# Kernel optimization log

Hardware: AMD Instinct MI355X
Metric: run time of the kernel (lower is better)

The kernel has to match this reference:

```python
import jax, jax.numpy as jnp
import numpy as np

N = 4096      # num_nodes
E = 16384     # edges per layer view
PHI = 64      # phi_dim
BETA = 0.5
EPS = 1e-8
LM = 1.0      # len(policy) per layer


def _mlp(x, w1, b1, w2, b2):
    # x: [E,1]; Linear(1,PHI) -> ReLU -> Linear(PHI,1)
    h = jax.nn.relu(x * w1[None, :] + b1[None, :])   # [E,PHI]
    return h @ w2[:, None] + b2                      # [E,1]


def setup_inputs() -> dict:
    key = jax.random.key(0)
    ks = jax.random.split(key, 16)
    inp = {
        "A": jax.random.uniform(ks[0], (N, N), dtype=jnp.float32),
        "src0": jax.random.randint(ks[1], (E,), 0, N),
        "dst0": jax.random.randint(ks[2], (E,), 0, N),
        "src1": jax.random.randint(ks[3], (E,), 0, N),
        "dst1": jax.random.randint(ks[4], (E,), 0, N),
        "f0": jax.random.normal(ks[5], (N, 1), dtype=jnp.float32),
        "f1": jax.random.normal(ks[6], (N, 1), dtype=jnp.float32),
        "phi1_w1": jax.random.normal(ks[7], (2, PHI), dtype=jnp.float32) * 0.5,
        "phi1_b1": jax.random.normal(ks[8], (2, PHI), dtype=jnp.float32) * 0.1,
        "phi1_w2": jax.random.normal(ks[9], (2, PHI), dtype=jnp.float32) * 0.5,
        "phi1_b2": jax.random.normal(ks[10], (2,), dtype=jnp.float32) * 0.1,
        "phi2_w1": jax.random.normal(ks[11], (2, PHI), dtype=jnp.float32) * 0.5,
        "phi2_b1": jax.random.normal(ks[12], (2, PHI), dtype=jnp.float32) * 0.1,
        "phi2_w2": jax.random.normal(ks[13], (2, PHI), dtype=jnp.float32) * 0.5,
        "phi2_b2": jax.random.normal(ks[14], (2,), dtype=jnp.float32) * 0.1,
    }
    return inp


def reference(A, src0, dst0, src1, dst1, f0, f1,
              phi1_w1, phi1_b1, phi1_w2, phi1_b2,
              phi2_w1, phi2_b1, phi2_w2, phi2_b2):
    # mean node struct feature across the two merged layer views: [N]
    f_mean = (0.5 * (f0 + f1))[:, 0]
    outs = []
    for lid, (src, dst) in enumerate([(src0, dst0), (src1, dst1)]):
        # gathered, feature-weighted adjacency rows: [E, N]
        mat_src = A[src] * f_mean[None, :]
        mat_dst = A[dst] * f_mean[None, :]
        # diag(mat_src @ mat_dst.T) == per-edge dot product: [E]
        out_struct = jnp.sum(mat_src * mat_dst, axis=-1)
        # random_fill with f_dropout=0 -> deterministic +eps, then row norms
        d_src = jnp.linalg.norm(mat_src + EPS, axis=-1)
        d_dst = jnp.linalg.norm(mat_dst + EPS, axis=-1)
        out_n = (out_struct / (d_src * d_dst))[:, None]      # [E,1]
        y1 = _mlp(out_n, phi1_w1[lid], phi1_b1[lid], phi1_w2[lid], phi1_b2[lid])
        sl1 = BETA * (y1 / LM)
        outs.append(_mlp(sl1, phi2_w1[lid], phi2_b1[lid], phi2_w2[lid], phi2_b2[lid]))
    return tuple(outs)
```

## Files before the change

kernel.cpp:

```cpp
#include <hip/hip_runtime.h>

#define N_NODES 4096
#define EDGES   16384
#define PHI     64
#define EPS_F   1e-8f
#define BETA_F  0.5f
#define NCHUNK  8
#define WCHUNK  512

__device__ __forceinline__ float wave_sum(float v) {
#pragma unroll
    for (int off = 32; off > 0; off >>= 1) v += __shfl_xor(v, off, 64);
    return v;
}

__device__ __forceinline__ unsigned int pack_bf16(float f) {
    unsigned int u = __float_as_uint(f);
    u += 0x7fffu + ((u >> 16) & 1u);
    return u >> 16;
}

__global__ void k_prep(const float* __restrict__ f0, const float* __restrict__ f1,
                       float* __restrict__ fm, float* __restrict__ wsq) {
    int i = blockIdx.x * blockDim.x + threadIdx.x;
    if (i < N_NODES) {
        float m = 0.5f * (f0[i] + f1[i]);
        fm[i]  = m;
        wsq[i] = m * m;
    }
}

__global__ void __launch_bounds__(256) k_rows_fast(const float* __restrict__ A,
                                                   const float* __restrict__ fm,
                                                   unsigned short* __restrict__ B,
                                                   float* __restrict__ dnorm) {
    int row = blockIdx.x;
    const float4* a4  = (const float4*)(A + (size_t)row * N_NODES);
    const float4* fm4 = (const float4*)fm;
    uint2* b2 = (uint2*)(B + (size_t)row * N_NODES);
    int t = threadIdx.x;
    float acc = 0.f;
#pragma unroll
    for (int i = 0; i < 4; ++i) {
        int idx = i * 256 + t;
        float4 a = a4[idx];
        float4 f = fm4[idx];
        float b0 = a.x * f.x, b1 = a.y * f.y, b2v = a.z * f.z, b3 = a.w * f.w;
        float e0 = b0 + EPS_F, e1 = b1 + EPS_F, e2 = b2v + EPS_F, e3 = b3 + EPS_F;
        acc += e0 * e0 + e1 * e1 + e2 * e2 + e3 * e3;
        uint2 p;
        p.x = (pack_bf16(b1) << 16) | pack_bf16(b0);
        p.y = (pack_bf16(b3) << 16) | pack_bf16(b2v);
        b2[idx] = p;
    }
    acc = wave_sum(acc);
    __shared__ float red[4];
    if ((t & 63) == 0) red[t >> 6] = acc;
    __syncthreads();
    if (t == 0) dnorm[row] = sqrtf(red[0] + red[1] + red[2] + red[3]);
}

__global__ void __launch_bounds__(256) k_rows_slow(const float* __restrict__ A,
                                                   const float* __restrict__ fm,
                                                   float* __restrict__ dnorm) {
    int row = blockIdx.x;
    const float4* a4  = (const float4*)(A + (size_t)row * N_NODES);
    const float4* fm4 = (const float4*)fm;
    int t = threadIdx.x;
    float acc = 0.f;
#pragma unroll
    for (int i = 0; i < 4; ++i) {
        int idx = i * 256 + t;
        float4 a = a4[idx];
        float4 f = fm4[idx];
        float e0 = a.x * f.x + EPS_F, e1 = a.y * f.y + EPS_F;
        float e2 = a.z * f.z + EPS_F, e3 = a.w * f.w + EPS_F;
        acc += e0 * e0 + e1 * e1 + e2 * e2 + e3 * e3;
    }
    acc = wave_sum(acc);
    __shared__ float red[4];
    if ((t & 63) == 0) red[t >> 6] = acc;
    __syncthreads();
    if (t == 0) dnorm[row] = sqrtf(red[0] + red[1] + red[2] + red[3]);
}

__device__ __forceinline__ void mlp_epilogue(float x, int lid, int e, int lane,
                                             const float* __restrict__ p1w1, const float* __restrict__ p1b1,
                                             const float* __restrict__ p1w2, const float* __restrict__ p1b2,
                                             const float* __restrict__ p2w1, const float* __restrict__ p2b1,
                                             const float* __restrict__ p2w2, const float* __restrict__ p2b2,
                                             float* __restrict__ out) {
    int wi = lid * PHI + lane;
    float h1 = fmaxf(fmaf(x, p1w1[wi], p1b1[wi]), 0.f);
    float y1 = wave_sum(h1 * p1w2[wi]) + p1b2[lid];
    float sl1 = BETA_F * y1;
    float h2 = fmaxf(fmaf(sl1, p2w1[wi], p2b1[wi]), 0.f);
    float y2 = wave_sum(h2 * p2w2[wi]) + p2b2[lid];
    if (lane == 0) out[lid * EDGES + e] = y2;
}

__global__ void __launch_bounds__(256) k_edges_chunk(
        const unsigned short* __restrict__ B,
        const int* __restrict__ src0, const int* __restrict__ dst0,
        const int* __restrict__ src1, const int* __restrict__ dst1,
        float* __restrict__ P) {
    int blk   = blockIdx.x;
    int chunk = blk & (NCHUNK - 1);
    int slot  = blk >> 3;
    int wave  = threadIdx.x >> 6;
    int lane  = threadIdx.x & 63;
    int ge0   = slot * 16 + wave * 4;
    const unsigned short* Bc = B + (size_t)chunk * WCHUNK;
#pragma unroll
    for (int k = 0; k < 4; ++k) {
        int ge  = ge0 + k;
        int lid = ge >> 14;
        int e   = ge & (EDGES - 1);
        int s = lid ? src1[e] : src0[e];
        int d = lid ? dst1[e] : dst0[e];
        uint4 us = *((const uint4*)(Bc + (size_t)s * N_NODES) + lane);
        uint4 ud = *((const uint4*)(Bc + (size_t)d * N_NODES) + lane);
        float acc = 0.f;
#define ACC_U(U, V)                                                    \
        {                                                              \
            float sl = __uint_as_float((U) << 16);                     \
            float sh = __uint_as_float((U) & 0xffff0000u);             \
            float dl = __uint_as_float((V) << 16);                     \
            float dh = __uint_as_float((V) & 0xffff0000u);             \
            acc = fmaf(sl, dl, acc);                                   \
            acc = fmaf(sh, dh, acc);                                   \
        }
        ACC_U(us.x, ud.x); ACC_U(us.y, ud.y); ACC_U(us.z, ud.z); ACC_U(us.w, ud.w);
#undef ACC_U
        acc = wave_sum(acc);
        if (lane == 0) P[(size_t)ge * NCHUNK + chunk] = acc;
    }
}

__global__ void __launch_bounds__(256) k_finish(
        const float* __restrict__ P, const float* __restrict__ dnorm,
        const int* __restrict__ src0, const int* __restrict__ dst0,
        const int* __restrict__ src1, const int* __restrict__ dst1,
        const float* __restrict__ p1w1, const float* __restrict__ p1b1,
        const float* __restrict__ p1w2, const float* __restrict__ p1b2,
        const float* __restrict__ p2w1, const float* __restrict__ p2b1,
        const float* __restrict__ p2w2, const float* __restrict__ p2b2,
        float* __restrict__ out) {
    int gw   = (int)((blockIdx.x * blockDim.x + threadIdx.x) >> 6);
    int lane = threadIdx.x & 63;
    int lid  = gw >> 14;
    int e    = gw & (EDGES - 1);
    int s = lid ? src1[e] : src0[e];
    int d = lid ? dst1[e] : dst0[e];
    float acc = 0.f;
#pragma unroll
    for (int c = 0; c < NCHUNK; ++c) acc += P[(size_t)gw * NCHUNK + c];
    float x = acc / (dnorm[s] * dnorm[d]);
    mlp_epilogue(x, lid, e, lane, p1w1, p1b1, p1w2, p1b2, p2w1, p2b1, p2w2, p2b2, out);
}

__global__ void __launch_bounds__(256) k_edges_fast(
        const unsigned short* __restrict__ B, const float* __restrict__ dnorm,
        const int* __restrict__ src0, const int* __restrict__ dst0,
        const int* __restrict__ src1, const int* __restrict__ dst1,
        const float* __restrict__ p1w1, const float* __restrict__ p1b1,
        const float* __restrict__ p1w2, const float* __restrict__ p1b2,
        const float* __restrict__ p2w1, const float* __restrict__ p2b1,
        const float* __restrict__ p2w2, const float* __restrict__ p2b2,
        float* __restrict__ out) {
    int gw   = (int)((blockIdx.x * blockDim.x + threadIdx.x) >> 6);
    int lane = threadIdx.x & 63;
    int lid  = gw >> 14;
    int e    = gw & (EDGES - 1);
    int s = lid ? src1[e] : src0[e];
    int d = lid ? dst1[e] : dst0[e];
    const uint4* rs = (const uint4*)(B + (size_t)s * N_NODES);
    const uint4* rd = (const uint4*)(B + (size_t)d * N_NODES);
    float acc = 0.f;
#pragma unroll
    for (int i = 0; i < 8; ++i) {
        uint4 us = rs[i * 64 + lane];
        uint4 ud = rd[i * 64 + lane];
#define ACC_U(U, V)                                                    \
        {                                                              \
            float sl = __uint_as_float((U) << 16);                     \
            float sh = __uint_as_float((U) & 0xffff0000u);             \
            float dl = __uint_as_float((V) << 16);                     \
            float dh = __uint_as_float((V) & 0xffff0000u);             \
            acc = fmaf(sl, dl, acc);                                   \
            acc = fmaf(sh, dh, acc);                                   \
        }
        ACC_U(us.x, ud.x); ACC_U(us.y, ud.y); ACC_U(us.z, ud.z); ACC_U(us.w, ud.w);
#undef ACC_U
    }
    acc = wave_sum(acc);
    float x = acc / (dnorm[s] * dnorm[d]);
    mlp_epilogue(x, lid, e, lane, p1w1, p1b1, p1w2, p1b2, p2w1, p2b1, p2w2, p2b2, out);
}

__global__ void __launch_bounds__(256) k_edges_slow(
        const float* __restrict__ A, const float* __restrict__ wsq,
        const float* __restrict__ dnorm,
        const int* __restrict__ src0, const int* __restrict__ dst0,
        const int* __restrict__ src1, const int* __restrict__ dst1,
        const float* __restrict__ p1w1, const float* __restrict__ p1b1,
        const float* __restrict__ p1w2, const float* __restrict__ p1b2,
        const float* __restrict__ p2w1, const float* __restrict__ p2b1,
        const float* __restrict__ p2w2, const float* __restrict__ p2b2,
        float* __restrict__ out) {
    __shared__ float wl[N_NODES];
    int t = threadIdx.x;
    const float4* w4 = (const float4*)wsq;
    float4* wl4 = (float4*)wl;
    for (int i = t; i < N_NODES / 4; i += 256) wl4[i] = w4[i];
    __syncthreads();

    int gw   = (int)((blockIdx.x * blockDim.x + t) >> 6);
    int lane = t & 63;
    int lid  = gw >> 14;
    int e    = gw & (EDGES - 1);
    int s = lid ? src1[e] : src0[e];
    int d = lid ? dst1[e] : dst0[e];
    const float4* rs = (const float4*)(A + (size_t)s * N_NODES);
    const float4* rd = (const float4*)(A + (size_t)d * N_NODES);
    float acc = 0.f;
#pragma unroll
    for (int i = 0; i < 16; ++i) {
        int idx = i * 64 + lane;
        float4 a = rs[idx];
        float4 b = rd[idx];
        float4 w = wl4[idx];
        acc = fmaf(a.x * b.x, w.x, acc);
        acc = fmaf(a.y * b.y, w.y, acc);
        acc = fmaf(a.z * b.z, w.z, acc);
        acc = fmaf(a.w * b.w, w.w, acc);
    }
    acc = wave_sum(acc);
    float x = acc / (dnorm[s] * dnorm[d]);
    mlp_epilogue(x, lid, e, lane, p1w1, p1b1, p1w2, p1b2, p2w1, p2b1, p2w2, p2b2, out);
}

extern "C" void kernel_launch(void* const* d_in, const int* in_sizes, int n_in,
                              void* d_out, int out_size, void* d_ws, size_t ws_size,
                              hipStream_t stream) {
    const float* A    = (const float*)d_in[0];
    const int*   src0 = (const int*)d_in[1];
    const int*   dst0 = (const int*)d_in[2];
    const int*   src1 = (const int*)d_in[3];
    const int*   dst1 = (const int*)d_in[4];
    const float* f0   = (const float*)d_in[5];
    const float* f1   = (const float*)d_in[6];
    const float* p1w1 = (const float*)d_in[7];
    const float* p1b1 = (const float*)d_in[8];
    const float* p1w2 = (const float*)d_in[9];
    const float* p1b2 = (const float*)d_in[10];
    const float* p2w1 = (const float*)d_in[11];
    const float* p2b1 = (const float*)d_in[12];
    const float* p2w2 = (const float*)d_in[13];
    const float* p2b2 = (const float*)d_in[14];
    float* out = (float*)d_out;

    float* ws  = (float*)d_ws;
    float* fm  = ws;
    float* wsq = ws + N_NODES;
    float* dn  = ws + 2 * N_NODES;
    float* P   = ws + 3 * N_NODES;
    unsigned short* Bnew = (unsigned short*)(P + NCHUNK * 2 * EDGES);
    unsigned short* Bold = (unsigned short*)(ws + 3 * N_NODES);

    size_t need_new = (3ull * N_NODES + (size_t)NCHUNK * 2 * EDGES) * 4
                      + (size_t)N_NODES * N_NODES * 2;
    size_t need_old = 3ull * N_NODES * 4 + (size_t)N_NODES * N_NODES * 2;

    k_prep<<<N_NODES / 256, 256, 0, stream>>>(f0, f1, fm, wsq);
    if (ws_size >= need_new) {
        k_rows_fast<<<N_NODES, 256, 0, stream>>>(A, fm, Bnew, dn);
        k_edges_chunk<<<(2 * EDGES * NCHUNK) / 16, 256, 0, stream>>>(
            Bnew, src0, dst0, src1, dst1, P);
        k_finish<<<(2 * EDGES * 64) / 256, 256, 0, stream>>>(
            P, dn, src0, dst0, src1, dst1,
            p1w1, p1b1, p1w2, p1b2, p2w1, p2b1, p2w2, p2b2, out);
    } else if (ws_size >= need_old) {
        k_rows_fast<<<N_NODES, 256, 0, stream>>>(A, fm, Bold, dn);
        k_edges_fast<<<(2 * EDGES * 64) / 256, 256, 0, stream>>>(
            Bold, dn, src0, dst0, src1, dst1,
            p1w1, p1b1, p1w2, p1b2, p2w1, p2b1, p2w2, p2b2, out);
    } else {
        k_rows_slow<<<N_NODES, 256, 0, stream>>>(A, fm, dn);
        k_edges_slow<<<(2 * EDGES * 64) / 256, 256, 0, stream>>>(
            A, wsq, dn, src0, dst0, src1, dst1,
            p1w1, p1b1, p1w2, p1b2, p2w1, p2b1, p2w2, p2b2, out);
    }
}
```

Before: 172.9 us.

## Fuse feature averaging into row pass and widen per-edge chunk work

The feature mean is now computed inside the row-scaling kernel, so the separate prep launch is dropped on the fast path. The chunked edge kernel now gives each 8-lane group one edge and has it load eight 16-byte vectors per endpoint row, so each wave covers 8 edges with more loads in flight. The final reduction becomes a 3-step shuffle instead of a full wave sum. The partial buffer is transposed to chunk-major order so both writes and the finish kernel's reads are contiguous. Register use rises from holding 16 uint4 values per thread, which may lower occupancy.

```diff
diff --git a/kernel.cpp b/kernel.cpp
--- a/kernel.cpp
+++ b/kernel.cpp
@@ -31,12 +31,14 @@
 }
 
 __global__ void __launch_bounds__(256) k_rows_fast(const float* __restrict__ A,
-                                                   const float* __restrict__ fm,
+                                                   const float* __restrict__ f0,
+                                                   const float* __restrict__ f1,
                                                    unsigned short* __restrict__ B,
                                                    float* __restrict__ dnorm) {
     int row = blockIdx.x;
     const float4* a4  = (const float4*)(A + (size_t)row * N_NODES);
-    const float4* fm4 = (const float4*)fm;
+    const float4* f04 = (const float4*)f0;
+    const float4* f14 = (const float4*)f1;
     uint2* b2 = (uint2*)(B + (size_t)row * N_NODES);
     int t = threadIdx.x;
     float acc = 0.f;
@@ -44,8 +46,11 @@
     for (int i = 0; i < 4; ++i) {
         int idx = i * 256 + t;
         float4 a = a4[idx];
-        float4 f = fm4[idx];
-        float b0 = a.x * f.x, b1 = a.y * f.y, b2v = a.z * f.z, b3 = a.w * f.w;
+        float4 fa = f04[idx];
+        float4 fb = f14[idx];
+        float fx = 0.5f * (fa.x + fb.x), fy = 0.5f * (fa.y + fb.y);
+        float fz = 0.5f * (fa.z + fb.z), fw = 0.5f * (fa.w + fb.w);
+        float b0 = a.x * fx, b1 = a.y * fy, b2v = a.z * fz, b3 = a.w * fw;
         float e0 = b0 + EPS_F, e1 = b1 + EPS_F, e2 = b2v + EPS_F, e3 = b3 + EPS_F;
         acc += e0 * e0 + e1 * e1 + e2 * e2 + e3 * e3;
         uint2 p;
@@ -109,18 +114,27 @@
     int slot  = blk >> 3;
     int wave  = threadIdx.x >> 6;
     int lane  = threadIdx.x & 63;
-    int ge0   = slot * 16 + wave * 4;
-    const unsigned short* Bc = B + (size_t)chunk * WCHUNK;
-#pragma unroll
-    for (int k = 0; k < 4; ++k) {
-        int ge  = ge0 + k;
-        int lid = ge >> 14;
-        int e   = ge & (EDGES - 1);
-        int s = lid ? src1[e] : src0[e];
-        int d = lid ? dst1[e] : dst0[e];
-        uint4 us = *((const uint4*)(Bc + (size_t)s * N_NODES) + lane);
-        uint4 ud = *((const uint4*)(Bc + (size_t)d * N_NODES) + lane);
-        float acc = 0.f;
+    int g     = lane >> 3;
+    int sub   = lane & 7;
+
+    int ge  = slot * 32 + wave * 8 + g;
+    int lid = ge >> 14;
+    int e   = ge & (EDGES - 1);
+    int s = lid ? src1[e] : src0[e];
+    int d = lid ? dst1[e] : dst0[e];
+
+    const uint4* rs = (const uint4*)(B + (size_t)s * N_NODES + chunk * WCHUNK);
+    const uint4* rd = (const uint4*)(B + (size_t)d * N_NODES + chunk * WCHUNK);
+
+    uint4 us[8], ud[8];
+#pragma unroll
+    for (int i = 0; i < 8; ++i) {
+        us[i] = rs[i * 8 + sub];
+        ud[i] = rd[i * 8 + sub];
+    }
+    float acc = 0.f;
+#pragma unroll
+    for (int i = 0; i < 8; ++i) {
 #define ACC_U(U, V)                                                    \
         {                                                              \
             float sl = __uint_as_float((U) << 16);                     \
@@ -130,11 +144,14 @@
             acc = fmaf(sl, dl, acc);                                   \
             acc = fmaf(sh, dh, acc);                                   \
         }
-        ACC_U(us.x, ud.x); ACC_U(us.y, ud.y); ACC_U(us.z, ud.z); ACC_U(us.w, ud.w);
+        ACC_U(us[i].x, ud[i].x); ACC_U(us[i].y, ud[i].y);
+        ACC_U(us[i].z, ud[i].z); ACC_U(us[i].w, ud[i].w);
 #undef ACC_U
-        acc = wave_sum(acc);
-        if (lane == 0) P[(size_t)ge * NCHUNK + chunk] = acc;
-    }
+    }
+    acc += __shfl_xor(acc, 1, 64);
+    acc += __shfl_xor(acc, 2, 64);
+    acc += __shfl_xor(acc, 4, 64);
+    if (sub == 0) P[(size_t)chunk * (2 * EDGES) + ge] = acc;
 }
 
 __global__ void __launch_bounds__(256) k_finish(
@@ -154,7 +171,7 @@
     int d = lid ? dst1[e] : dst0[e];
     float acc = 0.f;
 #pragma unroll
-    for (int c = 0; c < NCHUNK; ++c) acc += P[(size_t)gw * NCHUNK + c];
+    for (int c = 0; c < NCHUNK; ++c) acc += P[(size_t)c * (2 * EDGES) + gw];
     float x = acc / (dnorm[s] * dnorm[d]);
     mlp_epilogue(x, lid, e, lane, p1w1, p1b1, p1w2, p1b2, p2w1, p2b1, p2w2, p2b2, out);
 }
@@ -272,20 +289,21 @@
                       + (size_t)N_NODES * N_NODES * 2;
     size_t need_old = 3ull * N_NODES * 4 + (size_t)N_NODES * N_NODES * 2;
 
-    k_prep<<<N_NODES / 256, 256, 0, stream>>>(f0, f1, fm, wsq);
     if (ws_size >= need_new) {
-        k_rows_fast<<<N_NODES, 256, 0, stream>>>(A, fm, Bnew, dn);
-        k_edges_chunk<<<(2 * EDGES * NCHUNK) / 16, 256, 0, stream>>>(
+        k_rows_fast<<<N_NODES, 256, 0, stream>>>(A, f0, f1, Bnew, dn);
+        k_edges_chunk<<<(2 * EDGES * NCHUNK) / 32, 256, 0, stream>>>(
             Bnew, src0, dst0, src1, dst1, P);
         k_finish<<<(2 * EDGES * 64) / 256, 256, 0, stream>>>(
             P, dn, src0, dst0, src1, dst1,
             p1w1, p1b1, p1w2, p1b2, p2w1, p2b1, p2w2, p2b2, out);
     } else if (ws_size >= need_old) {
-        k_rows_fast<<<N_NODES, 256, 0, stream>>>(A, fm, Bold, dn);
+        k_prep<<<N_NODES / 256, 256, 0, stream>>>(f0, f1, fm, wsq);
+        k_rows_fast<<<N_NODES, 256, 0, stream>>>(A, f0, f1, Bold, dn);
         k_edges_fast<<<(2 * EDGES * 64) / 256, 256, 0, stream>>>(
             Bold, dn, src0, dst0, src1, dst1,
             p1w1, p1b1, p1w2, p1b2, p2w1, p2b1, p2w2, p2b2, out);
     } else {
+        k_prep<<<N_NODES / 256, 256, 0, stream>>>(f0, f1, fm, wsq);
         k_rows_slow<<<N_NODES, 256, 0, stream>>>(A, fm, dn);
         k_edges_slow<<<(2 * EDGES * 64) / 256, 256, 0, stream>>>(
             A, wsq, dn, src0, dst0, src1, dst1,
```

New measurement: 160.0 us. 7.5% less time.
